# Kernel tuning notes

Measured on AMD Instinct MI355X. Metric: run time of the kernel, lower is better.

The kernel has to match this reference:

```python
import jax, jax.numpy as jnp
import numpy as np

F = 16        # num_frames
K = 8         # num_tokens (top-k)
SIZE = 64     # basis size
PD = 256      # prompt_dim
ED = 768      # embed_dim
EPS = 1e-12

def _l2norm(v, axis=-1):
    n = jnp.sqrt(jnp.sum(v * v, axis=axis, keepdims=True))
    return v / jnp.maximum(n, EPS)

def setup_inputs() -> dict:
    key = jax.random.key(0)
    k1, k2, k3, k4 = jax.random.split(key, 4)
    B, N = 32, 197
    x = jax.random.normal(k1, (B, F * N, ED), dtype=jnp.float32)
    # prompt_values ~ U(-1, 1), shape [size, 1, prompt_dim]
    prompt_values = jax.random.uniform(k2, (SIZE, 1, PD), dtype=jnp.float32, minval=-1.0, maxval=1.0)
    # prompt_inproj: Linear(embed_dim, prompt_dim, bias=False)
    W_in = jax.random.normal(k3, (PD, ED), dtype=jnp.float32) * (1.0 / np.sqrt(ED))
    # prompt_outproj: Linear(prompt_dim, embed_dim, bias=False), kaiming fan_out
    W_out = jax.random.normal(k4, (ED, PD), dtype=jnp.float32) * np.sqrt(2.0 / ED)
    return {"x": x, "W_in": W_in, "W_out": W_out, "prompt_values": prompt_values}

def reference(x, W_in, W_out, prompt_values):
    B = x.shape[0]
    x = jax.lax.stop_gradient(x)                       # x.detach()
    xf = x.reshape(B, F, -1, ED).mean(axis=2)          # [B, F, ED]
    query = jnp.einsum('bfe,pe->bfp', xf, W_in)        # prompt_inproj
    BZ = B * F
    q = _l2norm(query.reshape(BZ, PD), axis=1)         # [BZ, PD]
    keys = _l2norm(prompt_values.mean(axis=1), axis=1) # [SIZE, PD]
    sim = q @ keys.T                                   # [BZ, SIZE]
    # eval routing: top-k by similarity (argsort descending [:, :k])
    _, idx = jax.lax.top_k(sim, K)                     # [BZ, K] int32
    prompts = prompt_values[idx.reshape(-1)].reshape(BZ, K, PD)
    prompts = _l2norm(prompts, axis=-1)
    sel_sim = jnp.take_along_axis(sim, idx, axis=1)    # [BZ, K]
    sel_key = keys[idx]                                # [BZ, K, PD]
    recon = jnp.einsum('bk,bkd->bd', sel_sim, sel_key) # [BZ, PD]
    diff = jnp.sum((recon - jax.lax.stop_gradient(q)) ** 2) / BZ
    ksim = jnp.sum(jnp.abs(keys @ keys.T - jnp.eye(SIZE, dtype=keys.dtype))) / BZ
    ps = diff + ksim
    # rearrange '(b f) p d -> b (f p) d' then outproj
    out_prompts = prompts.reshape(B, F * K, PD)
    out_prompts = jnp.einsum('bnd,ed->bne', out_prompts, W_out)  # [B, F*K, ED]
    ps_loss = jnp.zeros((1,), dtype=x.dtype) + ps * F
    return out_prompts, ps_loss
```

## Files before the change

### kernel.cpp

```cpp
#include <hip/hip_runtime.h>

#define Ff 16
#define Kk 8
#define SIZEk 64
#define PDd 256
#define EDd 768
#define Nn 197
#define BZz 512
#define NPROD 64
#define NMEAN 1536
#define RB  256
#define ED4 192
#define PD4 64
#define OUT_LOSS ((size_t)32 * 128 * EDd)
#define LOSS_SCALE (1.0f / 32.0f)
#define MAGIC 0x5A17EC0Du

__device__ __forceinline__ void acc4(float4& s, float4 a) {
    s.x += a.x; s.y += a.y; s.z += a.z; s.w += a.w;
}

__global__ __launch_bounds__(256, 4) void k_mean(const float4* __restrict__ x,
                                                 const float* __restrict__ Wout,
                                                 const float* __restrict__ pv,
                                                 float* __restrict__ keys,
                                                 float* __restrict__ KW,
                                                 unsigned* __restrict__ slots,
                                                 float4* __restrict__ xf,
                                                 float* __restrict__ out) {
    int blk = blockIdx.x, t = threadIdx.x;

    if (blk < NPROD) {
        __shared__ float ks[PDd];
        __shared__ float redp[4];
        __shared__ float s_norm;
        int s = blk;
        float v  = pv[(size_t)s * PDd + t];
        float sq = v * v;
        for (int o = 32; o > 0; o >>= 1) sq += __shfl_down(sq, o);
        if ((t & 63) == 0) redp[t >> 6] = sq;
        __syncthreads();
        if (t == 0) s_norm = fmaxf(sqrtf(redp[0] + redp[1] + redp[2] + redp[3]), 1e-12f);
        __syncthreads();
        float kv = v / s_norm;
        ks[t] = kv;
        keys[(size_t)s * PDd + t] = kv;
        __syncthreads();

        for (int r = 0; r < 3; r++) {
            int e = t + 256 * r;
            const float4* w  = (const float4*)(Wout + (size_t)e * PDd);
            const float4* k4 = (const float4*)ks;
            float d = 0.f;
            for (int i = 0; i < PD4; i++) {
                float4 wv = w[i]; float4 kvv = k4[i];
                d += wv.x * kvv.x + wv.y * kvv.y + wv.z * kvv.z + wv.w * kvv.w;
            }
            KW[(size_t)s * EDd + e] = d;
        }
        if (s == 0 && t == 0) out[OUT_LOSS] = 0.0f;
        __syncthreads();
        if (t == 0)
            __hip_atomic_store(&slots[s], MAGIC, __ATOMIC_RELEASE, __HIP_MEMORY_SCOPE_AGENT);

        if (t < SIZEk) {
            while (__hip_atomic_load(&slots[t], __ATOMIC_ACQUIRE, __HIP_MEMORY_SCOPE_AGENT)
                   != MAGIC)
                __builtin_amdgcn_s_sleep(8);
        }
        __syncthreads();
        if (t < SIZEk) {
            const float4* a = (const float4*)(keys + (size_t)s * PDd);
            const float4* b = (const float4*)(keys + (size_t)t * PDd);
            float d = 0.f;
            for (int c = 0; c < PD4; c++) {
                float4 av = a[c], bv = b[c];
                d += av.x * bv.x + av.y * bv.y + av.z * bv.z + av.w * bv.w;
            }
            float vv = fabsf(d - (s == t ? 1.0f : 0.0f));
            for (int o = 32; o > 0; o >>= 1) vv += __shfl_down(vv, o);
            if (t == 0) atomicAdd(out + OUT_LOSS, vv * LOSS_SCALE);
        }
        return;
    }

    int m  = blk - NPROD;
    int bz = m / 3;
    int c3 = m - bz * 3;
    int c = t & 63, g = t >> 6;
    const int STR = 4 * ED4;
    const float4* p = x + ((size_t)bz * Nn + g) * ED4 + c3 * 64 + c;
    float4 s = make_float4(0.f, 0.f, 0.f, 0.f);
    int cnt = (Nn - g + 3) >> 2;
    int j = 0;
    for (; j + 8 <= cnt; j += 8) {
        float4 a0 = p[(size_t)(j + 0) * STR], a1 = p[(size_t)(j + 1) * STR];
        float4 a2 = p[(size_t)(j + 2) * STR], a3 = p[(size_t)(j + 3) * STR];
        float4 a4 = p[(size_t)(j + 4) * STR], a5 = p[(size_t)(j + 5) * STR];
        float4 a6 = p[(size_t)(j + 6) * STR], a7 = p[(size_t)(j + 7) * STR];
        acc4(s, a0); acc4(s, a1); acc4(s, a2); acc4(s, a3);
        acc4(s, a4); acc4(s, a5); acc4(s, a6); acc4(s, a7);
    }
    for (; j < cnt; j++) acc4(s, p[(size_t)j * STR]);

    __shared__ float4 part[4][64];
    part[g][c] = s;
    __syncthreads();
    if (t < 64) {
        float4 a = part[0][t], b = part[1][t], d2 = part[2][t], e = part[3][t];
        const float inv = 1.0f / (float)Nn;
        float4 r;
        r.x = (a.x + b.x + d2.x + e.x) * inv;
        r.y = (a.y + b.y + d2.y + e.y) * inv;
        r.z = (a.z + b.z + d2.z + e.z) * inv;
        r.w = (a.w + b.w + d2.w + e.w) * inv;
        xf[(size_t)bz * ED4 + c3 * 64 + t] = r;
    }
}

__global__ __launch_bounds__(256, 2) void k_route(const float* __restrict__ Win,
                                                  const float* __restrict__ keys,
                                                  const float* __restrict__ KW,
                                                  const float4* __restrict__ xf,
                                                  float* __restrict__ out) {
    int blk = blockIdx.x, t = threadIdx.x;
    __shared__ float xs[2][EDd];
    __shared__ float qs[2][PDd];
    __shared__ int   s_idx[2][Kk];
    __shared__ float s_sim[2][Kk];
    __shared__ float red[2][4];
    int bz0 = blk * 2;

    {
        const float4* src = xf + (size_t)bz0 * ED4;
        for (int i = t; i < 2 * ED4; i += 256)
            ((float4*)xs)[i] = src[i];
    }
    __syncthreads();

    {
        const float4* w  = (const float4*)Win + (size_t)t * ED4;
        const float4* x0 = (const float4*)xs[0];
        const float4* x1 = (const float4*)xs[1];
        float d0a = 0.f, d0b = 0.f, d1a = 0.f, d1b = 0.f;
        for (int i = 0; i < ED4; i += 2) {
            float4 w0 = w[i],      w1 = w[i + 1];
            float4 u0 = x0[i],     u1 = x1[i];
            float4 u2 = x0[i + 1], u3 = x1[i + 1];
            d0a += w0.x * u0.x + w0.y * u0.y + w0.z * u0.z + w0.w * u0.w;
            d1a += w0.x * u1.x + w0.y * u1.y + w0.z * u1.z + w0.w * u1.w;
            d0b += w1.x * u2.x + w1.y * u2.y + w1.z * u2.z + w1.w * u2.w;
            d1b += w1.x * u3.x + w1.y * u3.y + w1.z * u3.z + w1.w * u3.w;
        }
        float d0 = d0a + d0b, d1 = d1a + d1b;
        float sq0 = d0 * d0, sq1 = d1 * d1;
        for (int o = 32; o > 0; o >>= 1) {
            sq0 += __shfl_down(sq0, o);
            sq1 += __shfl_down(sq1, o);
        }
        if ((t & 63) == 0) { red[0][t >> 6] = sq0; red[1][t >> 6] = sq1; }
        __syncthreads();
        float n0 = fmaxf(sqrtf(red[0][0] + red[0][1] + red[0][2] + red[0][3]), 1e-12f);
        float n1 = fmaxf(sqrtf(red[1][0] + red[1][1] + red[1][2] + red[1][3]), 1e-12f);
        qs[0][t] = d0 / n0;
        qs[1][t] = d1 / n1;
    }
    __syncthreads();

    if (t < 2 * SIZEk) {
        int row  = t >> 6;
        int lane = t & 63;
        const float4* kr = (const float4*)(keys + (size_t)lane * PDd);
        const float4* qr = (const float4*)qs[row];
        float d = 0.f;
        for (int c = 0; c < PD4; c++) {
            float4 a = kr[c], b = qr[c];
            d += a.x * b.x + a.y * b.y + a.z * b.z + a.w * b.w;
        }
        float v = d;
        for (int k = 0; k < Kk; k++) {
            float mv = v; int mi = lane;
            for (int o = 32; o > 0; o >>= 1) {
                float ov = __shfl_xor(mv, o);
                int   oi = __shfl_xor(mi, o);
                if (ov > mv || (ov == mv && oi < mi)) { mv = ov; mi = oi; }
            }
            if (lane == 0) { s_idx[row][k] = mi; s_sim[row][k] = mv; }
            if (lane == mi) v = -3e38f;
        }
    }
    __syncthreads();

    {
        float r0 = 0.f, r1 = 0.f;
        for (int k = 0; k < Kk; k++) {
            r0 += s_sim[0][k] * keys[(size_t)s_idx[0][k] * PDd + t];
            r1 += s_sim[1][k] * keys[(size_t)s_idx[1][k] * PDd + t];
        }
        float e0 = r0 - qs[0][t];
        float e1 = r1 - qs[1][t];
        float sq = e0 * e0 + e1 * e1;
        for (int o = 32; o > 0; o >>= 1) sq += __shfl_down(sq, o);
        if ((t & 63) == 0) red[0][t >> 6] = sq;
        __syncthreads();
        if (t == 0) atomicAdd(out + OUT_LOSS,
                              (red[0][0] + red[0][1] + red[0][2] + red[0][3]) * LOSS_SCALE);
    }

    float4* orow = (float4*)out + (size_t)bz0 * Kk * ED4;
    for (int i = t; i < 2 * Kk * ED4; i += 256) {
        int which = i / ED4;
        int e4    = i - which * ED4;
        int idx   = s_idx[which >> 3][which & 7];
        orow[i] = ((const float4*)(KW + (size_t)idx * EDd))[e4];
    }
}

extern "C" void kernel_launch(void* const* d_in, const int* in_sizes, int n_in,
                              void* d_out, int out_size, void* d_ws, size_t ws_size,
                              hipStream_t stream) {
    const float* x    = (const float*)d_in[0];
    const float* Win  = (const float*)d_in[1];
    const float* Wout = (const float*)d_in[2];
    const float* pv   = (const float*)d_in[3];
    float* out = (float*)d_out;
    float* ws  = (float*)d_ws;

    float*    keys  = ws;
    float*    KW    = ws + 16384;
    unsigned* slots = (unsigned*)(ws + 65536);
    float*    xf    = ws + 65600;

    k_mean<<<NPROD + NMEAN, 256, 0, stream>>>((const float4*)x, Wout, pv,
                                              keys, KW, slots, (float4*)xf, out);
    k_route<<<RB, 256, 0, stream>>>(Win, keys, KW, (const float4*)xf, out);
}
```

Before: 510.5 us.

## Fuse mean and routing kernels into one launch with per-block ready flags

```diff
diff --git a/kernel.cpp b/kernel.cpp
--- a/kernel.cpp
+++ b/kernel.cpp
@@ -20,14 +20,16 @@
     s.x += a.x; s.y += a.y; s.z += a.z; s.w += a.w;
 }
 
-__global__ __launch_bounds__(256, 4) void k_mean(const float4* __restrict__ x,
-                                                 const float* __restrict__ Wout,
-                                                 const float* __restrict__ pv,
-                                                 float* __restrict__ keys,
-                                                 float* __restrict__ KW,
-                                                 unsigned* __restrict__ slots,
-                                                 float4* __restrict__ xf,
-                                                 float* __restrict__ out) {
+__global__ __launch_bounds__(256, 4) void k_all(const float4* __restrict__ x,
+                                                const float* __restrict__ Win,
+                                                const float* __restrict__ Wout,
+                                                const float* __restrict__ pv,
+                                                float* __restrict__ keys,
+                                                float* __restrict__ KW,
+                                                unsigned* __restrict__ slots,
+                                                unsigned* __restrict__ dflags,
+                                                float4* __restrict__ xf,
+                                                float* __restrict__ out) {
     int blk = blockIdx.x, t = threadIdx.x;
 
     if (blk < NPROD) {
@@ -84,52 +86,62 @@
         return;
     }
 
-    int m  = blk - NPROD;
-    int bz = m / 3;
-    int c3 = m - bz * 3;
-    int c = t & 63, g = t >> 6;
-    const int STR = 4 * ED4;
-    const float4* p = x + ((size_t)bz * Nn + g) * ED4 + c3 * 64 + c;
-    float4 s = make_float4(0.f, 0.f, 0.f, 0.f);
-    int cnt = (Nn - g + 3) >> 2;
-    int j = 0;
-    for (; j + 8 <= cnt; j += 8) {
-        float4 a0 = p[(size_t)(j + 0) * STR], a1 = p[(size_t)(j + 1) * STR];
-        float4 a2 = p[(size_t)(j + 2) * STR], a3 = p[(size_t)(j + 3) * STR];
-        float4 a4 = p[(size_t)(j + 4) * STR], a5 = p[(size_t)(j + 5) * STR];
-        float4 a6 = p[(size_t)(j + 6) * STR], a7 = p[(size_t)(j + 7) * STR];
-        acc4(s, a0); acc4(s, a1); acc4(s, a2); acc4(s, a3);
-        acc4(s, a4); acc4(s, a5); acc4(s, a6); acc4(s, a7);
-    }
-    for (; j < cnt; j++) acc4(s, p[(size_t)j * STR]);
-
-    __shared__ float4 part[4][64];
-    part[g][c] = s;
-    __syncthreads();
-    if (t < 64) {
-        float4 a = part[0][t], b = part[1][t], d2 = part[2][t], e = part[3][t];
-        const float inv = 1.0f / (float)Nn;
-        float4 r;
-        r.x = (a.x + b.x + d2.x + e.x) * inv;
-        r.y = (a.y + b.y + d2.y + e.y) * inv;
-        r.z = (a.z + b.z + d2.z + e.z) * inv;
-        r.w = (a.w + b.w + d2.w + e.w) * inv;
-        xf[(size_t)bz * ED4 + c3 * 64 + t] = r;
-    }
-}
-
-__global__ __launch_bounds__(256, 2) void k_route(const float* __restrict__ Win,
-                                                  const float* __restrict__ keys,
-                                                  const float* __restrict__ KW,
-                                                  const float4* __restrict__ xf,
-                                                  float* __restrict__ out) {
-    int blk = blockIdx.x, t = threadIdx.x;
+    if (blk < NPROD + NMEAN) {
+        int m  = blk - NPROD;
+        int bz = m / 3;
+        int c3 = m - bz * 3;
+        int c = t & 63, g = t >> 6;
+        const int STR = 4 * ED4;
+        const float4* p = x + ((size_t)bz * Nn + g) * ED4 + c3 * 64 + c;
+        float4 s = make_float4(0.f, 0.f, 0.f, 0.f);
+        int cnt = (Nn - g + 3) >> 2;
+        int j = 0;
+        for (; j + 8 <= cnt; j += 8) {
+            float4 a0 = p[(size_t)(j + 0) * STR], a1 = p[(size_t)(j + 1) * STR];
+            float4 a2 = p[(size_t)(j + 2) * STR], a3 = p[(size_t)(j + 3) * STR];
+            float4 a4 = p[(size_t)(j + 4) * STR], a5 = p[(size_t)(j + 5) * STR];
+            float4 a6 = p[(size_t)(j + 6) * STR], a7 = p[(size_t)(j + 7) * STR];
+            acc4(s, a0); acc4(s, a1); acc4(s, a2); acc4(s, a3);
+            acc4(s, a4); acc4(s, a5); acc4(s, a6); acc4(s, a7);
+        }
+        for (; j < cnt; j++) acc4(s, p[(size_t)j * STR]);
+
+        __shared__ float4 part[4][64];
+        part[g][c] = s;
+        __syncthreads();
+        if (t < 64) {
+            float4 a = part[0][t], b = part[1][t], d2 = part[2][t], e = part[3][t];
+            const float inv = 1.0f / (float)Nn;
+            float4 r;
+            r.x = (a.x + b.x + d2.x + e.x) * inv;
+            r.y = (a.y + b.y + d2.y + e.y) * inv;
+            r.z = (a.z + b.z + d2.z + e.z) * inv;
+            r.w = (a.w + b.w + d2.w + e.w) * inv;
+            xf[(size_t)bz * ED4 + c3 * 64 + t] = r;
+        }
+        __syncthreads();
+        if (t == 0)
+            __hip_atomic_store(&dflags[m], MAGIC, __ATOMIC_RELEASE, __HIP_MEMORY_SCOPE_AGENT);
+        return;
+    }
+
     __shared__ float xs[2][EDd];
     __shared__ float qs[2][PDd];
     __shared__ int   s_idx[2][Kk];
     __shared__ float s_sim[2][Kk];
     __shared__ float red[2][4];
-    int bz0 = blk * 2;
+    int bz0 = (blk - NPROD - NMEAN) * 2;
+
+    if (t < SIZEk) {
+        while (__hip_atomic_load(&slots[t], __ATOMIC_ACQUIRE, __HIP_MEMORY_SCOPE_AGENT)
+               != MAGIC)
+            __builtin_amdgcn_s_sleep(8);
+    } else if (t < SIZEk + 6) {
+        while (__hip_atomic_load(&dflags[bz0 * 3 + (t - SIZEk)], __ATOMIC_ACQUIRE,
+                                 __HIP_MEMORY_SCOPE_AGENT) != MAGIC)
+            __builtin_amdgcn_s_sleep(8);
+    }
+    __syncthreads();
 
     {
         const float4* src = xf + (size_t)bz0 * ED4;
@@ -226,12 +238,13 @@
     float* out = (float*)d_out;
     float* ws  = (float*)d_ws;
 
-    float*    keys  = ws;
-    float*    KW    = ws + 16384;
-    unsigned* slots = (unsigned*)(ws + 65536);
-    float*    xf    = ws + 65600;
-
-    k_mean<<<NPROD + NMEAN, 256, 0, stream>>>((const float4*)x, Wout, pv,
-                                              keys, KW, slots, (float4*)xf, out);
-    k_route<<<RB, 256, 0, stream>>>(Win, keys, KW, (const float4*)xf, out);
+    float*    keys   = ws;
+    float*    KW     = ws + 16384;
+    unsigned* slots  = (unsigned*)(ws + 65536);
+    unsigned* dflags = (unsigned*)(ws + 65600);
+    float*    xf     = ws + 67136;
+
+    k_all<<<NPROD + NMEAN + RB, 256, 0, stream>>>((const float4*)x, Win, Wout, pv,
+                                                  keys, KW, slots, dflags,
+                                                  (float4*)xf, out);
 }
```

Result: slower. 787.4 us (+54.2%).

## Stream contiguous row halves in mean reduction and combine partials in route kernel

Applied to the files above, without the earlier changes.

```diff
diff --git a/kernel.cpp b/kernel.cpp
--- a/kernel.cpp
+++ b/kernel.cpp
@@ -1,14 +1,12 @@
 #include <hip/hip_runtime.h>
 
-#define Ff 16
 #define Kk 8
 #define SIZEk 64
 #define PDd 256
 #define EDd 768
 #define Nn 197
-#define BZz 512
 #define NPROD 64
-#define NMEAN 1536
+#define NMEAN 1024
 #define RB  256
 #define ED4 192
 #define PD4 64
@@ -26,7 +24,7 @@
                                                  float* __restrict__ keys,
                                                  float* __restrict__ KW,
                                                  unsigned* __restrict__ slots,
-                                                 float4* __restrict__ xf,
+                                                 float4* __restrict__ xfp,
                                                  float* __restrict__ out) {
     int blk = blockIdx.x, t = threadIdx.x;
 
@@ -84,44 +82,57 @@
         return;
     }
 
-    int m  = blk - NPROD;
-    int bz = m / 3;
-    int c3 = m - bz * 3;
-    int c = t & 63, g = t >> 6;
-    const int STR = 4 * ED4;
-    const float4* p = x + ((size_t)bz * Nn + g) * ED4 + c3 * 64 + c;
-    float4 s = make_float4(0.f, 0.f, 0.f, 0.f);
-    int cnt = (Nn - g + 3) >> 2;
+    int m    = blk - NPROD;
+    int bz   = m >> 1;
+    int half = m & 1;
+    int rowstart = half ? 99 : 0;
+    int nrows    = half ? 98 : 99;
+    const float4* base = x + ((size_t)bz * Nn + rowstart) * ED4;
+    const int total = nrows * ED4;
+    const int jfull = total >> 8;
+    const int jmain = jfull - (jfull % 6);
+
+    float4 a0 = make_float4(0.f, 0.f, 0.f, 0.f);
+    float4 a1 = a0, a2 = a0;
     int j = 0;
-    for (; j + 8 <= cnt; j += 8) {
-        float4 a0 = p[(size_t)(j + 0) * STR], a1 = p[(size_t)(j + 1) * STR];
-        float4 a2 = p[(size_t)(j + 2) * STR], a3 = p[(size_t)(j + 3) * STR];
-        float4 a4 = p[(size_t)(j + 4) * STR], a5 = p[(size_t)(j + 5) * STR];
-        float4 a6 = p[(size_t)(j + 6) * STR], a7 = p[(size_t)(j + 7) * STR];
-        acc4(s, a0); acc4(s, a1); acc4(s, a2); acc4(s, a3);
-        acc4(s, a4); acc4(s, a5); acc4(s, a6); acc4(s, a7);
-    }
-    for (; j < cnt; j++) acc4(s, p[(size_t)j * STR]);
-
-    __shared__ float4 part[4][64];
-    part[g][c] = s;
-    __syncthreads();
-    if (t < 64) {
-        float4 a = part[0][t], b = part[1][t], d2 = part[2][t], e = part[3][t];
-        const float inv = 1.0f / (float)Nn;
-        float4 r;
-        r.x = (a.x + b.x + d2.x + e.x) * inv;
-        r.y = (a.y + b.y + d2.y + e.y) * inv;
-        r.z = (a.z + b.z + d2.z + e.z) * inv;
-        r.w = (a.w + b.w + d2.w + e.w) * inv;
-        xf[(size_t)bz * ED4 + c3 * 64 + t] = r;
+    for (; j < jmain; j += 6) {
+        const float4* p = base + (size_t)j * 256 + t;
+        float4 v0 = p[0 * 256], v1 = p[1 * 256], v2 = p[2 * 256];
+        float4 v3 = p[3 * 256], v4 = p[4 * 256], v5 = p[5 * 256];
+        acc4(a0, v0); acc4(a1, v1); acc4(a2, v2);
+        acc4(a0, v3); acc4(a1, v4); acc4(a2, v5);
+    }
+    {
+        int f = j * 256 + t;
+        if (f < total) acc4(a0, base[f]); f += 256;
+        if (f < total) acc4(a1, base[f]); f += 256;
+        if (f < total) acc4(a2, base[f]); f += 256;
+        if (f < total) acc4(a0, base[f]);
+    }
+
+    __shared__ float4 part[4][ED4];
+    {
+        int k  = t >> 6;
+        int c0 = t & 255 % 192;
+        c0 = t % 192;
+        int c1 = (t + 64) % 192;
+        int c2 = (t + 128) % 192;
+        part[k][c0] = a0;
+        part[k][c1] = a1;
+        part[k][c2] = a2;
+    }
+    __syncthreads();
+    if (t < ED4) {
+        float4 s = part[0][t];
+        acc4(s, part[1][t]); acc4(s, part[2][t]); acc4(s, part[3][t]);
+        xfp[(size_t)(bz * 2 + half) * ED4 + t] = s;
     }
 }
 
 __global__ __launch_bounds__(256, 2) void k_route(const float* __restrict__ Win,
                                                   const float* __restrict__ keys,
                                                   const float* __restrict__ KW,
-                                                  const float4* __restrict__ xf,
+                                                  const float4* __restrict__ xfp,
                                                   float* __restrict__ out) {
     int blk = blockIdx.x, t = threadIdx.x;
     __shared__ float xs[2][EDd];
@@ -132,9 +143,20 @@
     int bz0 = blk * 2;
 
     {
-        const float4* src = xf + (size_t)bz0 * ED4;
-        for (int i = t; i < 2 * ED4; i += 256)
-            ((float4*)xs)[i] = src[i];
+        const float inv = 1.0f / (float)Nn;
+        for (int i = t; i < 2 * ED4; i += 256) {
+            int row = i / ED4;
+            int e4  = i - row * ED4;
+            const float4* src = xfp + (size_t)(bz0 + row) * 2 * ED4;
+            float4 A = src[e4];
+            float4 B = src[ED4 + e4];
+            float4 r;
+            r.x = (A.x + B.x) * inv;
+            r.y = (A.y + B.y) * inv;
+            r.z = (A.z + B.z) * inv;
+            r.w = (A.w + B.w) * inv;
+            ((float4*)xs)[i] = r;
+        }
     }
     __syncthreads();
 
@@ -229,9 +251,9 @@
     float*    keys  = ws;
     float*    KW    = ws + 16384;
     unsigned* slots = (unsigned*)(ws + 65536);
-    float*    xf    = ws + 65600;
+    float*    xfp   = ws + 65600;
 
     k_mean<<<NPROD + NMEAN, 256, 0, stream>>>((const float4*)x, Wout, pv,
-                                              keys, KW, slots, (float4*)xf, out);
-    k_route<<<RB, 256, 0, stream>>>(Win, keys, KW, (const float4*)xf, out);
-}
+                                              keys, KW, slots, (float4*)xfp, out);
+    k_route<<<RB, 256, 0, stream>>>(Win, keys, KW, (const float4*)xfp, out);
+}
```

Result: no change. 516.0 us (+1.1%).
